# Optimization experiments

Hardware: AMD Instinct MI355X
Metric: run time of the kernel (lower is better)

The kernel has to match this reference:

```python
import jax, jax.numpy as jnp
import numpy as np

EMBED_DIM = 384
NUM_HEADS = 6
EPS = 1e-5

def _conv_proj(x, w_dw, gamma, beta, mean, var, stride):
    # x: [B,H,W,C]; depthwise 3x3 conv (groups=C), pad 1, then BN (inference), then flatten HW.
    C = x.shape[-1]
    y = jax.lax.conv_general_dilated(
        x, w_dw, window_strides=(stride, stride), padding=[(1, 1), (1, 1)],
        dimension_numbers=("NHWC", "HWIO", "NHWC"), feature_group_count=C)
    y = (y - mean) * jax.lax.rsqrt(var + EPS) * gamma + beta
    B, H, W, Cc = y.shape
    return y.reshape(B, H * W, Cc)

def _heads(x):
    # [B, L, C] -> [B, nH, L, hd]
    B, L, C = x.shape
    hd = C // NUM_HEADS
    return x.reshape(B, L, NUM_HEADS, hd).transpose(0, 2, 1, 3)

def setup_inputs() -> dict:
    key = jax.random.key(0)
    ks = jax.random.split(key, 20)
    B, H, W, C = 64, 28, 28, EMBED_DIM
    inp = {
        "hidden_state": jax.random.normal(ks[0], (B, 1 + H * W, C), dtype=jnp.float32),
        "height": H,
        "width": W,
    }
    std = 0.02
    for i, p in enumerate(("q", "k", "v")):
        inp[f"w_dw_{p}"] = jax.random.normal(ks[1 + i], (3, 3, 1, C), dtype=jnp.float32) * std
        inp[f"bn_gamma_{p}"] = jnp.ones((C,), jnp.float32) + 0.1 * jax.random.normal(ks[4 + i], (C,))
        inp[f"bn_beta_{p}"] = 0.1 * jax.random.normal(ks[7 + i], (C,))
        inp[f"bn_mean_{p}"] = 0.1 * jax.random.normal(ks[10 + i], (C,))
        inp[f"bn_var_{p}"] = jnp.ones((C,), jnp.float32) + 0.1 * jax.random.uniform(ks[13 + i], (C,))
        inp[f"W_{p}"] = jax.random.normal(ks[16 + i], (C, C), dtype=jnp.float32) * std
        inp[f"b_{p}"] = jnp.zeros((C,), jnp.float32)
    return inp

def reference(hidden_state, height, width,
              w_dw_q, bn_gamma_q, bn_beta_q, bn_mean_q, bn_var_q, W_q, b_q,
              w_dw_k, bn_gamma_k, bn_beta_k, bn_mean_k, bn_var_k, W_k, b_k,
              w_dw_v, bn_gamma_v, bn_beta_v, bn_mean_v, bn_var_v, W_v, b_v):
    B, _, C = hidden_state.shape
    scale = C ** (-0.5)  # note: embed_dim**-0.5, as in the source
    cls_token = hidden_state[:, :1]
    x = hidden_state[:, 1:].reshape(B, height, width, C)

    q = _conv_proj(x, w_dw_q, bn_gamma_q, bn_beta_q, bn_mean_q, bn_var_q, stride=1)
    k = _conv_proj(x, w_dw_k, bn_gamma_k, bn_beta_k, bn_mean_k, bn_var_k, stride=2)
    v = _conv_proj(x, w_dw_v, bn_gamma_v, bn_beta_v, bn_mean_v, bn_var_v, stride=2)

    q = jnp.concatenate((cls_token, q), axis=1)
    k = jnp.concatenate((cls_token, k), axis=1)
    v = jnp.concatenate((cls_token, v), axis=1)

    q = _heads(q @ W_q + b_q)  # [B,h,Lq,d]
    k = _heads(k @ W_k + b_k)  # [B,h,Lk,d]
    v = _heads(v @ W_v + b_v)

    scores = jnp.einsum("bhqd,bhkd->bhqk", q, k) * scale
    probs = jax.nn.softmax(scores, axis=-1)
    ctx = jnp.einsum("bhqk,bhkd->bhqd", probs, v)
    Lq = ctx.shape[2]
    return ctx.transpose(0, 2, 1, 3).reshape(B, Lq, C)
```

## Files before the change

### kernel.cpp

```cpp
#include <hip/hip_runtime.h>
#include <hip/hip_bf16.h>

#define C_DIM 384
#define BATCH 64
#define LQ 785
#define LK 197
#define NHEADS 6
#define HDIM 64
#define QTILES 785
#define KTILES 197
#define KPAD 208

typedef __hip_bfloat16 bf16;
typedef __attribute__((ext_vector_type(8))) short short8;
typedef __attribute__((ext_vector_type(4))) float float4v;

__device__ __forceinline__ float bf2f(bf16 x) { return __bfloat162float(x); }
__device__ __forceinline__ bf16 f2bf(float x) { return __float2bfloat16(x); }
__device__ __forceinline__ float lo16f(unsigned int u) { return __uint_as_float(u << 16); }
__device__ __forceinline__ float hi16f(unsigned int u) { return __uint_as_float(u & 0xffff0000u); }
__device__ __forceinline__ unsigned short bfb(float x) {
    union { bf16 h; unsigned short s; } u; u.h = f2bf(x); return u.s;
}
__device__ __forceinline__ unsigned int pk2(float a, float b) {
    return ((unsigned int)bfb(b) << 16) | bfb(a);
}

template<bool F32>
__device__ __forceinline__ float ldx(const void* p, size_t i) {
    if constexpr (F32) return ((const float*)p)[i];
    else return bf2f(((const bf16*)p)[i]);
}
template<bool F32>
__device__ __forceinline__ void stx(void* p, size_t i, float v) {
    if constexpr (F32) ((float*)p)[i] = v;
    else ((bf16*)p)[i] = f2bf(v);
}
template<bool F32>
__device__ __forceinline__ void ld4(const void* p, size_t i, float* o) {
    if constexpr (F32) {
        float4 v = *(const float4*)((const float*)p + i);
        o[0] = v.x; o[1] = v.y; o[2] = v.z; o[3] = v.w;
    } else {
        uint2 u = *(const uint2*)((const bf16*)p + i);
        o[0] = lo16f(u.x); o[1] = hi16f(u.x); o[2] = lo16f(u.y); o[3] = hi16f(u.y);
    }
}
template<bool F32>
__device__ __forceinline__ void ld2(const void* p, size_t i, float* o) {
    if constexpr (F32) {
        float2 v = *(const float2*)((const float*)p + i);
        o[0] = v.x; o[1] = v.y;
    } else {
        unsigned int u = *(const unsigned int*)((const bf16*)p + i);
        o[0] = lo16f(u); o[1] = hi16f(u);
    }
}

__global__ void detect_kernel(const void* varq, int* flag) {
    const unsigned short* u = (const unsigned short*)varq;
    int votes = 0;
    #pragma unroll
    for (int i = 0; i < 4; ++i) {
        float b = __uint_as_float(((unsigned int)u[2 * i]) << 16);
        votes += (b > 0.5f && b < 2.0f) ? 1 : 0;
    }
    *flag = (votes == 4) ? 1 : 0;
}

template<bool F32>
__global__ __launch_bounds__(256) void repack_kernel(const int* __restrict__ flagp,
    const void* __restrict__ W0, const void* __restrict__ W1, const void* __restrict__ W2,
    bf16* __restrict__ dst)
{
    if (*flagp != (F32 ? 0 : 1)) return;
    const void* W = blockIdx.y == 0 ? W0 : (blockIdx.y == 1 ? W1 : W2);
    bf16* d = dst + (size_t)blockIdx.y * (C_DIM * C_DIM);
    int idx = blockIdx.x * 256 + threadIdx.x;
    int k = idx / C_DIM, nc = idx - k * C_DIM;
    int nt = nc >> 4, n = nc & 15, kt = k >> 5, q = (k >> 3) & 3, j = k & 7;
    d[(size_t)((((nt * 12 + kt) * 4 + q) * 16 + n) * 8 + j)] = f2bf(ldx<F32>(W, idx));
}

template<bool F32>
__device__ __forceinline__ void foldw(const void* __restrict__ wdw,
    const void* __restrict__ gamma, const void* __restrict__ beta,
    const void* __restrict__ mean,  const void* __restrict__ var,
    int c0, float w[9][2], float sh[2])
{
    float g[2], be[2], mu[2], vv[2];
    ld2<F32>(gamma, c0, g); ld2<F32>(beta, c0, be);
    ld2<F32>(mean,  c0, mu); ld2<F32>(var,  c0, vv);
    float sc[2];
    #pragma unroll
    for (int i = 0; i < 2; ++i) {
        sc[i] = g[i] * rsqrtf(vv[i] + 1e-5f);
        sh[i] = be[i] - mu[i] * sc[i];
    }
    #pragma unroll
    for (int p = 0; p < 9; ++p) {
        float t[2];
        ld2<F32>(wdw, (size_t)p * C_DIM + c0, t);
        w[p][0] = t[0] * sc[0];
        w[p][1] = t[1] * sc[1];
    }
}

template<int OJH, bool F32>
__device__ __forceinline__ void conv_quad(int b, int oik, int c2,
    const void* __restrict__ hs,
    const void* wq_, const void* gq, const void* beq, const void* muq, const void* vaq,
    const void* wk_, const void* gk, const void* bek, const void* muk, const void* vak,
    const void* wv_, const void* gv, const void* bev, const void* muv, const void* vav,
    bf16* __restrict__ qa, bf16* __restrict__ ka, bf16* __restrict__ va)
{
    int c0 = c2 * 2;
    float wq[9][2], wk[9][2], wv[9][2], shq[2], shk[2], shv[2];
    foldw<F32>(wq_, gq, beq, muq, vaq, c0, wq, shq);
    foldw<F32>(wk_, gk, bek, muk, vak, c0, wk, shk);
    foldw<F32>(wv_, gv, bev, muv, vav, c0, wv, shv);

    size_t hb = (size_t)b * (LQ * C_DIM);
    int i0 = 2 * oik - 1;
    bool rv[4];
    #pragma unroll
    for (int ri = 0; ri < 4; ++ri) rv[ri] = ((unsigned)(i0 + ri)) < 28u;

    float xw[4][3][2];
    constexpr int JJ0 = 14 * OJH - 1;

    int rq0 = b * LQ + 1 + 2 * oik * 28;
    int rq1 = rq0 + 28;
    int rk  = b * LK + 1 + oik * 14;

    #pragma unroll
    for (int s = 0; s < 16; ++s) {
        const int jj = JJ0 + s;
        const int sl = ((jj % 3) + 3) % 3;
        const bool cval = (jj >= 0) && (jj < 28);
        #pragma unroll
        for (int ri = 0; ri < 4; ++ri) {
            if (cval && rv[ri])
                ld2<F32>(hs, hb + (size_t)(1 + (i0 + ri) * 28 + jj) * C_DIM + c0, xw[ri][sl]);
            else { xw[ri][sl][0] = 0.f; xw[ri][sl][1] = 0.f; }
        }
        if (s >= 2) {
            const int jc = jj - 1;
            float a0[2] = {}, a1[2] = {};
            #pragma unroll
            for (int di = 0; di < 3; ++di)
                #pragma unroll
                for (int dj = 0; dj < 3; ++dj) {
                    const int s2 = (((jc - 1 + dj) % 3) + 3) % 3;
                    const int t = di * 3 + dj;
                    a0[0] = fmaf(xw[di][s2][0],     wq[t][0], a0[0]);
                    a0[1] = fmaf(xw[di][s2][1],     wq[t][1], a0[1]);
                    a1[0] = fmaf(xw[di + 1][s2][0], wq[t][0], a1[0]);
                    a1[1] = fmaf(xw[di + 1][s2][1], wq[t][1], a1[1]);
                }
            *(unsigned int*)&qa[(size_t)(rq0 + jc) * C_DIM + c0] = pk2(a0[0] + shq[0], a0[1] + shq[1]);
            *(unsigned int*)&qa[(size_t)(rq1 + jc) * C_DIM + c0] = pk2(a1[0] + shq[0], a1[1] + shq[1]);
            if ((jc & 1) == 0) {
                float k0[2] = {}, v0[2] = {};
                #pragma unroll
                for (int di = 0; di < 3; ++di)
                    #pragma unroll
                    for (int dj = 0; dj < 3; ++dj) {
                        const int s2 = (((jc - 1 + dj) % 3) + 3) % 3;
                        const int t = di * 3 + dj;
                        k0[0] = fmaf(xw[di][s2][0], wk[t][0], k0[0]);
                        k0[1] = fmaf(xw[di][s2][1], wk[t][1], k0[1]);
                        v0[0] = fmaf(xw[di][s2][0], wv[t][0], v0[0]);
                        v0[1] = fmaf(xw[di][s2][1], wv[t][1], v0[1]);
                    }
                int ro = rk + (jc >> 1);
                *(unsigned int*)&ka[(size_t)ro * C_DIM + c0] = pk2(k0[0] + shk[0], k0[1] + shk[1]);
                *(unsigned int*)&va[(size_t)ro * C_DIM + c0] = pk2(v0[0] + shv[0], v0[1] + shv[1]);
            }
        }
    }
}

#define CONV4_BLOCKS 960
template<bool F32>
__global__ __launch_bounds__(384) void conv4_kernel(
    const int* __restrict__ flagp, const void* __restrict__ hs,
    const void* wq, const void* gq, const void* beq, const void* muq, const void* vaq,
    const void* wk, const void* gk, const void* bek, const void* muk, const void* vak,
    const void* wv, const void* gv, const void* bev, const void* muv, const void* vav,
    bf16* __restrict__ qa, bf16* __restrict__ ka, bf16* __restrict__ va)
{
    if (*flagp != (F32 ? 0 : 1)) return;
    int bid = blockIdx.x;
    int tid = threadIdx.x;
    if (bid < 896) {
        int w = (bid & 7) * 112 + (bid >> 3);
        int b = w / 14, oik = w - b * 14;
        int c2 = tid % 192, ojh = tid / 192;
        if (ojh == 0)
            conv_quad<0, F32>(b, oik, c2, hs, wq, gq, beq, muq, vaq,
                              wk, gk, bek, muk, vak, wv, gv, bev, muv, vav, qa, ka, va);
        else
            conv_quad<1, F32>(b, oik, c2, hs, wq, gq, beq, muq, vaq,
                              wk, gk, bek, muk, vak, wv, gv, bev, muv, vav, qa, ka, va);
    } else {
        int b = bid - 896;
        if (tid < 192) {
            int c0 = tid * 2;
            float v2[2];
            ld2<F32>(hs, (size_t)b * (LQ * C_DIM) + c0, v2);
            unsigned int pk = pk2(v2[0], v2[1]);
            *(unsigned int*)&qa[(size_t)(b * LQ) * C_DIM + c0] = pk;
            *(unsigned int*)&ka[(size_t)(b * LK) * C_DIM + c0] = pk;
            *(unsigned int*)&va[(size_t)(b * LK) * C_DIM + c0] = pk;
        }
    }
}

template<bool F32>
__global__ __launch_bounds__(512) void gemm_frag_kernel(
    const int* __restrict__ flagp,
    const bf16* __restrict__ qa, const bf16* __restrict__ ka, const bf16* __restrict__ va,
    const bf16* __restrict__ wrep,
    const void* __restrict__ b_q, const void* __restrict__ b_k, const void* __restrict__ b_v,
    void* __restrict__ outq, bf16* __restrict__ kbuf, bf16* __restrict__ vbuf)
{
    if (*flagp != (F32 ? 0 : 1)) return;

    int bidx = blockIdx.x;
    const bf16* A; const bf16* wr; const void* bias; int tile, mode;
    if (bidx < QTILES)                { mode = 0; tile = bidx;                  A = qa; wr = wrep;                          bias = b_q; }
    else if (bidx < QTILES + KTILES)  { mode = 1; tile = bidx - QTILES;         A = ka; wr = wrep + (size_t)C_DIM * C_DIM;     bias = b_k; }
    else                              { mode = 2; tile = bidx - QTILES - KTILES; A = va; wr = wrep + (size_t)2 * C_DIM * C_DIM; bias = b_v; }

    const bf16* Abase = A + (size_t)tile * (64 * C_DIM);
    const short8* wf = (const short8*)wr;
    int tid = threadIdx.x;
    int lane = tid & 63, wave = tid >> 6;
    int mrow = lane & 15, quad = lane >> 4;
    float4v acc[4][3] = {};

    #pragma unroll 2
    for (int kt = 0; kt < 12; ++kt) {
        short8 a[4];
        #pragma unroll
        for (int mt = 0; mt < 4; ++mt)
            a[mt] = *(const short8*)(Abase + (size_t)(mt * 16 + mrow) * C_DIM + (kt * 4 + quad) * 8);
        #pragma unroll
        for (int nt = 0; nt < 3; ++nt) {
            short8 bfrag = wf[(size_t)((wave * 3 + nt) * 12 + kt) * 64 + lane];
            #pragma unroll
            for (int mt = 0; mt < 4; ++mt)
                acc[mt][nt] = __builtin_amdgcn_mfma_f32_16x16x32_bf16(a[mt], bfrag, acc[mt][nt], 0, 0, 0);
        }
    }

    #pragma unroll
    for (int nt = 0; nt < 3; ++nt) {
        int col = wave * 48 + nt * 16 + mrow;
        float bb = ldx<F32>(bias, col);
        #pragma unroll
        for (int mt = 0; mt < 4; ++mt) {
            int row = tile * 64 + mt * 16 + quad * 4;
            #pragma unroll
            for (int r2 = 0; r2 < 4; ++r2) {
                float v = acc[mt][nt][r2] + bb;
                size_t o = (size_t)(row + r2) * C_DIM + col;
                if (mode == 0)      stx<F32>(outq, o, v);
                else if (mode == 1) kbuf[o] = f2bf(v);
                else                vbuf[o] = f2bf(v);
            }
        }
    }
}

__global__ __launch_bounds__(256) void vt_transpose_kernel(
    const bf16* __restrict__ v, bf16* __restrict__ vt)
{
    __shared__ unsigned short t[64][66];
    int bid = blockIdx.x;
    int ct = bid % 6; int tmp = bid / 6;
    int kt = tmp % 4; int b = tmp / 4;
    int k0 = kt * 64, c0 = ct * 64;
    int tid = threadIdx.x;

    for (int e = tid; e < 64 * 32; e += 256) {
        int r = e >> 5, c2 = e & 31;
        int k = k0 + r;
        unsigned int val = 0;
        if (k < LK) val = *(const unsigned int*)(v + ((size_t)b * LK + k) * C_DIM + c0 + c2 * 2);
        *(unsigned int*)&t[r][c2 * 2] = val;
    }
    __syncthreads();

    for (int e = tid; e < 64 * 32; e += 256) {
        int c = e >> 5, r2 = e & 31;
        int k = k0 + r2 * 2;
        if (k < KPAD) {
            unsigned int val = ((unsigned int)t[r2 * 2 + 1][c] << 16) | t[r2 * 2][c];
            *(unsigned int*)&vt[((size_t)(b * C_DIM + c0 + c)) * KPAD + k] = val;
        }
    }
}

template<int L, int OW, int STRIDE, bool F32, bool OF32>
__global__ __launch_bounds__(256) void fused_proj_kernel(
    const int* __restrict__ flagp,
    const void* __restrict__ hs, const void* __restrict__ wdw,
    const void* __restrict__ gamma, const void* __restrict__ beta,
    const void* __restrict__ mean,  const void* __restrict__ var,
    const bf16* __restrict__ Wrep,  const void* __restrict__ bias,
    void* __restrict__ O)
{
    if (*flagp != (F32 ? 0 : 1)) return;

    __shared__ bf16 A_s[64 * C_DIM];
    __shared__ float sc[C_DIM];
    __shared__ float sh[C_DIM];
    int tid = threadIdx.x;
    int m0 = blockIdx.x * 64;

    for (int c = tid; c < C_DIM; c += 256) {
        float s = ldx<F32>(gamma, c) * rsqrtf(ldx<F32>(var, c) + 1e-5f);
        sc[c] = s;
        sh[c] = ldx<F32>(beta, c) - ldx<F32>(mean, c) * s;
    }
    __syncthreads();

    for (int e = tid; e < 64 * 96; e += 256) {
        int m = e / 96;
        int c = (e - m * 96) * 4;
        int r = m0 + m;
        int b = r / L;
        int l = r - b * L;
        size_t hb = (size_t)b * (LQ * C_DIM);
        float v[4];
        if (l == 0) {
            ld4<F32>(hs, hb + c, v);
        } else {
            int p = l - 1;
            int oi = p / OW;
            int oj = p - oi * OW;
            float a0 = 0.f, a1 = 0.f, a2 = 0.f, a3 = 0.f;
            #pragma unroll
            for (int di = 0; di < 3; ++di) {
                int ii = oi * STRIDE - 1 + di;
                if (ii < 0 || ii >= 28) continue;
                #pragma unroll
                for (int dj = 0; dj < 3; ++dj) {
                    int jj = oj * STRIDE - 1 + dj;
                    if (jj < 0 || jj >= 28) continue;
                    float x[4], w[4];
                    ld4<F32>(hs, hb + (size_t)(1 + ii * 28 + jj) * C_DIM + c, x);
                    ld4<F32>(wdw, (size_t)(di * 3 + dj) * C_DIM + c, w);
                    a0 = fmaf(x[0], w[0], a0); a1 = fmaf(x[1], w[1], a1);
                    a2 = fmaf(x[2], w[2], a2); a3 = fmaf(x[3], w[3], a3);
                }
            }
            v[0] = a0 * sc[c + 0] + sh[c + 0];
            v[1] = a1 * sc[c + 1] + sh[c + 1];
            v[2] = a2 * sc[c + 2] + sh[c + 2];
            v[3] = a3 * sc[c + 3] + sh[c + 3];
        }
        int kt = c >> 5, q = (c >> 3) & 3, j = c & 7;
        int ofs = ((kt * 4 + q) * 64 + m) * 8 + j;
        ushort4 st = { bfb(v[0]), bfb(v[1]), bfb(v[2]), bfb(v[3]) };
        *(ushort4*)&A_s[ofs] = st;
    }
    __syncthreads();

    int lane = tid & 63, wave = tid >> 6;
    int mrow = lane & 15, quad = lane >> 4;
    float4v acc[4][6] = {};
    const short8* as = (const short8*)A_s;
    const short8* wr = (const short8*)Wrep;

    for (int kt = 0; kt < 12; ++kt) {
        short8 a[4];
        #pragma unroll
        for (int mt = 0; mt < 4; ++mt)
            a[mt] = as[(kt * 4 + quad) * 64 + mt * 16 + mrow];
        #pragma unroll
        for (int nt = 0; nt < 6; ++nt) {
            int ntg = wave * 6 + nt;
            short8 bfrag = wr[(size_t)(ntg * 12 + kt) * 64 + lane];
            #pragma unroll
            for (int mt = 0; mt < 4; ++mt)
                acc[mt][nt] = __builtin_amdgcn_mfma_f32_16x16x32_bf16(a[mt], bfrag, acc[mt][nt], 0, 0, 0);
        }
    }

    #pragma unroll
    for (int nt = 0; nt < 6; ++nt) {
        int col = wave * 96 + nt * 16 + mrow;
        float bb = ldx<F32>(bias, col);
        #pragma unroll
        for (int mt = 0; mt < 4; ++mt) {
            int row = m0 + mt * 16 + quad * 4;
            #pragma unroll
            for (int r2 = 0; r2 < 4; ++r2)
                stx<OF32>(O, (size_t)(row + r2) * C_DIM + col, acc[mt][nt][r2] + bb);
        }
    }
}

template<bool F32>
__global__ __launch_bounds__(256) void attn_vt_kernel(
    const int* __restrict__ flagp,
    const bf16* __restrict__ kg,
    const bf16* __restrict__ vt_g,
    void* __restrict__ qo)
{
    if (*flagp != (F32 ? 0 : 1)) return;

    __shared__ unsigned short Kf[8 * 2 * 64 * 8];
    __shared__ unsigned short Vt[64 * 128];
    __shared__ unsigned short Ps[4 * 16 * 128];

    int tid = threadIdx.x;
    int lane = tid & 63, wave = tid >> 6;
    int m = lane & 15, quad = lane >> 4;
    int bid = blockIdx.x;
    int qb = bid % 13;
    int bh = bid / 13;
    int h = bh % NHEADS, b = bh / NHEADS;
    int qbase = qb * 64 + wave * 16;

    int rev4m = ((m & 1) << 3) | ((m & 2) << 1) | ((m & 4) >> 1) | ((m & 8) >> 3);
    int revr[4];
    #pragma unroll
    for (int r = 0; r < 4; ++r) {
        int rr = quad * 4 + r;
        revr[r] = ((rr & 1) << 3) | ((rr & 2) << 1) | ((rr & 4) >> 1) | ((rr & 8) >> 3);
    }

    int qrow = min(qbase + m, LQ - 1);
    size_t qoff = ((size_t)b * LQ + qrow) * C_DIM + h * HDIM;
    short8 aq[2];
    #pragma unroll
    for (int ks = 0; ks < 2; ++ks) {
        float t[8];
        ld4<F32>(qo, qoff + ks * 32 + quad * 8, t);
        ld4<F32>(qo, qoff + ks * 32 + quad * 8 + 4, t + 4);
        short8 f;
        #pragma unroll
        for (int j = 0; j < 8; ++j) f[j] = (short)bfb(t[j]);
        aq[ks] = f;
    }

    const float scale = 0.05103103630798287f;
    float4v ctx[4] = {};
    float lsum4[4] = {};
    size_t kvbase = (size_t)b * LK * C_DIM + h * HDIM;
    size_t vtbase = (size_t)(b * C_DIM + h * HDIM) * KPAD;

    for (int c = 0; c < 2; ++c) {
        int c0 = c * 128;
        for (int e = tid; e < 1024; e += 256) {
            int col = e >> 3, d8 = e & 7;
            int gcol = c0 + col;
            uint4 val = {0, 0, 0, 0};
            if (gcol < LK) val = *(const uint4*)(kg + kvbase + (size_t)gcol * C_DIM + d8 * 8);
            int nt = col >> 4, n = col & 15, ks = d8 >> 2, q = d8 & 3;
            *(uint4*)&Kf[((nt * 2 + ks) * 64 + q * 16 + n) * 8] = val;
        }
        for (int e = tid; e < 1024; e += 256) {
            int d = e >> 4, kc = e & 15;
            uint4 val = {0, 0, 0, 0};
            if (c0 + kc * 8 < KPAD)
                val = *(const uint4*)(vt_g + vtbase + (size_t)d * KPAD + c0 + kc * 8);
            *(uint4*)&Vt[(d << 7) + ((kc ^ (d & 15)) << 3)] = val;
        }
        __syncthreads();

        const short8* kf = (const short8*)Kf;
        unsigned short* pw = Ps + wave * (16 * 128);
        int ntmax = (c == 0) ? 8 : 5;
        for (int nt = 0; nt < ntmax; ++nt) {
            float4v s = {0.f, 0.f, 0.f, 0.f};
            #pragma unroll
            for (int ks = 0; ks < 2; ++ks)
                s = __builtin_amdgcn_mfma_f32_16x16x32_bf16(aq[ks], kf[(nt * 2 + ks) * 64 + lane], s, 0, 0, 0);
            int coln = c0 + nt * 16 + m;
            bool valid = coln < LK;
            int chb = nt * 2 + (m >> 3);
            int sub = m & 7;
            #pragma unroll
            for (int r = 0; r < 4; ++r) {
                float pv = valid ? __expf(s[r] * scale) : 0.f;
                lsum4[r] += pv;
                pw[(((quad * 4 + r)) << 7) + ((chb ^ revr[r]) << 3) + sub] = bfb(pv);
            }
        }
        if (c == 1) {
            int sub = m & 7;
            #pragma unroll
            for (int nt = 5; nt < 8; ++nt) {
                int chb = nt * 2 + (m >> 3);
                #pragma unroll
                for (int r = 0; r < 4; ++r)
                    pw[(((quad * 4 + r)) << 7) + ((chb ^ revr[r]) << 3) + sub] = 0;
            }
        }

        const short8* vts = (const short8*)Vt;
        const short8* pf = (const short8*)Ps;
        #pragma unroll
        for (int ks = 0; ks < 4; ++ks) {
            short8 ap = pf[wave * 256 + (m << 4) + ((ks * 4 + quad) ^ rev4m)];
            #pragma unroll
            for (int ntv = 0; ntv < 4; ++ntv) {
                short8 bf_ = vts[((ntv * 16 + m) << 4) + ((ks * 4 + quad) ^ m)];
                ctx[ntv] = __builtin_amdgcn_mfma_f32_16x16x32_bf16(ap, bf_, ctx[ntv], 0, 0, 0);
            }
        }
        __syncthreads();
    }

    float inv[4];
    #pragma unroll
    for (int r = 0; r < 4; ++r) {
        float t = lsum4[r];
        t += __shfl_xor(t, 1);
        t += __shfl_xor(t, 2);
        t += __shfl_xor(t, 4);
        t += __shfl_xor(t, 8);
        inv[r] = 1.f / t;
    }
    #pragma unroll
    for (int ntv = 0; ntv < 4; ++ntv) {
        #pragma unroll
        for (int r = 0; r < 4; ++r) {
            int row = qbase + quad * 4 + r;
            if (row < LQ)
                stx<F32>(qo, ((size_t)b * LQ + row) * C_DIM + h * HDIM + ntv * 16 + m, ctx[ntv][r] * inv[r]);
        }
    }
}

template<bool F32>
__global__ __launch_bounds__(256) void attn_kernel(
    const int* __restrict__ flagp,
    const bf16* __restrict__ kg,
    const bf16* __restrict__ vg,
    void* __restrict__ qo)
{
    if (*flagp != (F32 ? 0 : 1)) return;

    __shared__ unsigned short Kf[8 * 2 * 64 * 8];
    __shared__ unsigned short Vf[4 * 4 * 64 * 8];
    __shared__ unsigned short Ps[4 * 16 * 136];

    int tid = threadIdx.x;
    int lane = tid & 63, wave = tid >> 6;
    int m = lane & 15, quad = lane >> 4;
    int bid = blockIdx.x;
    int qb = bid % 13;
    int bh = bid / 13;
    int h = bh % NHEADS, b = bh / NHEADS;
    int qbase = qb * 64 + wave * 16;

    int qrow = min(qbase + m, LQ - 1);
    size_t qoff = ((size_t)b * LQ + qrow) * C_DIM + h * HDIM;
    short8 aq[2];
    #pragma unroll
    for (int ks = 0; ks < 2; ++ks) {
        float t[8];
        ld4<F32>(qo, qoff + ks * 32 + quad * 8, t);
        ld4<F32>(qo, qoff + ks * 32 + quad * 8 + 4, t + 4);
        short8 f;
        #pragma unroll
        for (int j = 0; j < 8; ++j) f[j] = (short)bfb(t[j]);
        aq[ks] = f;
    }

    const float scale = 0.05103103630798287f;
    float4v ctx[4] = {};
    float lsum4[4] = {};
    size_t kvbase = (size_t)b * LK * C_DIM + h * HDIM;

    for (int c = 0; c < 2; ++c) {
        int c0 = c * 128;
        for (int e = tid; e < 1024; e += 256) {
            int col = e >> 3, d8 = e & 7;
            int gcol = c0 + col;
            uint4 val = {0, 0, 0, 0};
            if (gcol < LK) val = *(const uint4*)(kg + kvbase + (size_t)gcol * C_DIM + d8 * 8);
            int nt = col >> 4, n = col & 15, ks = d8 >> 2, q = d8 & 3;
            *(uint4*)&Kf[((nt * 2 + ks) * 64 + q * 16 + n) * 8] = val;
        }
        for (int e = tid; e < 1024; e += 256) {
            int p = e >> 3, d8 = e & 7;
            int gp = c0 + p;
            int ks = p >> 5, q = (p >> 3) & 3, j = p & 7;
            int ntv = d8 >> 1, nl0 = (d8 & 1) * 8;
            if (gp < LK) {
                union { uint4 u; unsigned short s[8]; } val;
                val.u = *(const uint4*)(vg + kvbase + (size_t)gp * C_DIM + d8 * 8);
                #pragma unroll
                for (int i = 0; i < 8; ++i)
                    Vf[((ntv * 4 + ks) * 64 + q * 16 + nl0 + i) * 8 + j] = val.s[i];
            } else {
                #pragma unroll
                for (int i = 0; i < 8; ++i)
                    Vf[((ntv * 4 + ks) * 64 + q * 16 + nl0 + i) * 8 + j] = 0;
            }
        }
        __syncthreads();

        const short8* kf = (const short8*)Kf;
        unsigned short* pw = Ps + wave * (16 * 136);
        int ntmax = (c == 0) ? 8 : 5;
        for (int nt = 0; nt < ntmax; ++nt) {
            float4v s = {0.f, 0.f, 0.f, 0.f};
            #pragma unroll
            for (int ks = 0; ks < 2; ++ks)
                s = __builtin_amdgcn_mfma_f32_16x16x32_bf16(aq[ks], kf[(nt * 2 + ks) * 64 + lane], s, 0, 0, 0);
            int coln = c0 + nt * 16 + m;
            bool valid = coln < LK;
            #pragma unroll
            for (int r = 0; r < 4; ++r) {
                float pv = valid ? __expf(s[r] * scale) : 0.f;
                lsum4[r] += pv;
                pw[(quad * 4 + r) * 136 + nt * 16 + m] = bfb(pv);
            }
        }
        if (c == 1) {
            #pragma unroll
            for (int nt = 5; nt < 8; ++nt)
                #pragma unroll
                for (int r = 0; r < 4; ++r)
                    pw[(quad * 4 + r) * 136 + nt * 16 + m] = 0;
        }

        const short8* vf = (const short8*)Vf;
        const short8* pf = (const short8*)Ps;
        #pragma unroll
        for (int ks = 0; ks < 4; ++ks) {
            short8 ap = pf[wave * 272 + m * 17 + ks * 4 + quad];
            #pragma unroll
            for (int ntv = 0; ntv < 4; ++ntv)
                ctx[ntv] = __builtin_amdgcn_mfma_f32_16x16x32_bf16(ap, vf[(ntv * 4 + ks) * 64 + lane], ctx[ntv], 0, 0, 0);
        }
        __syncthreads();
    }

    float inv[4];
    #pragma unroll
    for (int r = 0; r < 4; ++r) {
        float t = lsum4[r];
        t += __shfl_xor(t, 1);
        t += __shfl_xor(t, 2);
        t += __shfl_xor(t, 4);
        t += __shfl_xor(t, 8);
        inv[r] = 1.f / t;
    }
    #pragma unroll
    for (int ntv = 0; ntv < 4; ++ntv) {
        #pragma unroll
        for (int r = 0; r < 4; ++r) {
            int row = qbase + quad * 4 + r;
            if (row < LQ)
                stx<F32>(qo, ((size_t)b * LQ + row) * C_DIM + h * HDIM + ntv * 16 + m, ctx[ntv][r] * inv[r]);
        }
    }
}

extern "C" void kernel_launch(void* const* d_in, const int* in_sizes, int n_in,
                              void* d_out, int out_size, void* d_ws, size_t ws_size,
                              hipStream_t stream)
{
    const void* hs    = d_in[0];
    const void* wdw_q = d_in[3];
    const void* g_q   = d_in[4];
    const void* be_q  = d_in[5];
    const void* mu_q  = d_in[6];
    const void* va_q  = d_in[7];
    const void* W_q   = d_in[8];
    const void* b_q   = d_in[9];
    const void* wdw_k = d_in[10];
    const void* g_k   = d_in[11];
    const void* be_k  = d_in[12];
    const void* mu_k  = d_in[13];
    const void* va_k  = d_in[14];
    const void* W_k   = d_in[15];
    const void* b_k   = d_in[16];
    const void* wdw_v = d_in[17];
    const void* g_v   = d_in[18];
    const void* be_v  = d_in[19];
    const void* mu_v  = d_in[20];
    const void* va_v  = d_in[21];
    const void* W_v   = d_in[22];
    const void* b_v   = d_in[23];

    const size_t QA = (size_t)QTILES * 24576;
    const size_t KA = (size_t)KTILES * 24576;
    const size_t NEED_BIG = 16 + 2 * (3 * (size_t)C_DIM * C_DIM + QA + 4 * KA);

    int*  flag = (int*)d_ws;
    bf16* wrep = (bf16*)((char*)d_ws + 16);
    bf16* wrq  = wrep;
    bf16* wrk  = wrep + (size_t)C_DIM * C_DIM;
    bf16* wrv  = wrep + (size_t)2 * C_DIM * C_DIM;

    detect_kernel<<<1, 1, 0, stream>>>(va_q, flag);
    repack_kernel<false><<<dim3(576, 3), 256, 0, stream>>>(flag, W_q, W_k, W_v, wrep);
    repack_kernel<true ><<<dim3(576, 3), 256, 0, stream>>>(flag, W_q, W_k, W_v, wrep);

    if (ws_size >= NEED_BIG) {
        bf16* qa    = wrep + (size_t)3 * C_DIM * C_DIM;
        bf16* ka    = qa + QA;
        bf16* vaa   = ka + KA;
        bf16* kbuf  = vaa + KA;
        bf16* vbuf  = kbuf + KA;
        bf16* vbuft = qa;

        conv4_kernel<false><<<CONV4_BLOCKS, 384, 0, stream>>>(flag, hs,
            wdw_q, g_q, be_q, mu_q, va_q, wdw_k, g_k, be_k, mu_k, va_k,
            wdw_v, g_v, be_v, mu_v, va_v, qa, ka, vaa);
        conv4_kernel<true ><<<CONV4_BLOCKS, 384, 0, stream>>>(flag, hs,
            wdw_q, g_q, be_q, mu_q, va_q, wdw_k, g_k, be_k, mu_k, va_k,
            wdw_v, g_v, be_v, mu_v, va_v, qa, ka, vaa);

        gemm_frag_kernel<false><<<QTILES + 2 * KTILES, 512, 0, stream>>>(flag,
            qa, ka, vaa, wrep, b_q, b_k, b_v, d_out, kbuf, vbuf);
        gemm_frag_kernel<true ><<<QTILES + 2 * KTILES, 512, 0, stream>>>(flag,
            qa, ka, vaa, wrep, b_q, b_k, b_v, d_out, kbuf, vbuf);

        vt_transpose_kernel<<<BATCH * 24, 256, 0, stream>>>(vbuf, vbuft);

        attn_vt_kernel<false><<<384 * 13, 256, 0, stream>>>(flag, kbuf, vbuft, d_out);
        attn_vt_kernel<true ><<<384 * 13, 256, 0, stream>>>(flag, kbuf, vbuft, d_out);
    } else {
        bf16* kbuf = wrep + (size_t)3 * C_DIM * C_DIM;
        bf16* vbuf = kbuf + (size_t)BATCH * LK * C_DIM;

        fused_proj_kernel<LQ, 28, 1, false, false><<<LQ, 256, 0, stream>>>(flag, hs, wdw_q, g_q, be_q, mu_q, va_q, wrq, b_q, d_out);
        fused_proj_kernel<LQ, 28, 1, true,  true ><<<LQ, 256, 0, stream>>>(flag, hs, wdw_q, g_q, be_q, mu_q, va_q, wrq, b_q, d_out);
        fused_proj_kernel<LK, 14, 2, false, false><<<LK, 256, 0, stream>>>(flag, hs, wdw_k, g_k, be_k, mu_k, va_k, wrk, b_k, kbuf);
        fused_proj_kernel<LK, 14, 2, true,  false><<<LK, 256, 0, stream>>>(flag, hs, wdw_k, g_k, be_k, mu_k, va_k, wrk, b_k, kbuf);
        fused_proj_kernel<LK, 14, 2, false, false><<<LK, 256, 0, stream>>>(flag, hs, wdw_v, g_v, be_v, mu_v, va_v, wrv, b_v, vbuf);
        fused_proj_kernel<LK, 14, 2, true,  false><<<LK, 256, 0, stream>>>(flag, hs, wdw_v, g_v, be_v, mu_v, va_v, wrv, b_v, vbuf);

        attn_kernel<false><<<384 * 13, 256, 0, stream>>>(flag, kbuf, vbuf, d_out);
        attn_kernel<true ><<<384 * 13, 256, 0, stream>>>(flag, kbuf, vbuf, d_out);
    }
}
```

Measured before the change: 385.2 us.

## Stage GEMM A tile in swizzled LDS and merge dtype variants into one launch

Each 512-thread block now loads its 64x384 bf16 A tile into shared memory once, using a swizzled layout, before the MFMA loop. Previously all 8 waves re-read the same A fragments directly from global memory. The two templated launches (f32 and bf16 paths, one of which exited early) become a single launch that branches on the flag at runtime, removing one kernel launch. In exchange the kernel uses 48KB of LDS per block, which can limit how many blocks fit per CU, and adds a barrier.

```diff
diff --git a/kernel.cpp b/kernel.cpp
--- a/kernel.cpp
+++ b/kernel.cpp
@@ -217,16 +217,16 @@
     }
 }
 
-template<bool F32>
-__global__ __launch_bounds__(512) void gemm_frag_kernel(
+__global__ __launch_bounds__(512) void gemm_lds_kernel(
     const int* __restrict__ flagp,
     const bf16* __restrict__ qa, const bf16* __restrict__ ka, const bf16* __restrict__ va,
     const bf16* __restrict__ wrep,
     const void* __restrict__ b_q, const void* __restrict__ b_k, const void* __restrict__ b_v,
     void* __restrict__ outq, bf16* __restrict__ kbuf, bf16* __restrict__ vbuf)
 {
-    if (*flagp != (F32 ? 0 : 1)) return;
-
+    __shared__ bf16 A_s[64 * C_DIM];
+
+    const bool f32 = (*flagp == 0);
     int bidx = blockIdx.x;
     const bf16* A; const bf16* wr; const void* bias; int tile, mode;
     if (bidx < QTILES)                { mode = 0; tile = bidx;                  A = qa; wr = wrep;                          bias = b_q; }
@@ -234,10 +234,28 @@
     else                              { mode = 2; tile = bidx - QTILES - KTILES; A = va; wr = wrep + (size_t)2 * C_DIM * C_DIM; bias = b_v; }
 
     const bf16* Abase = A + (size_t)tile * (64 * C_DIM);
-    const short8* wf = (const short8*)wr;
     int tid = threadIdx.x;
     int lane = tid & 63, wave = tid >> 6;
     int mrow = lane & 15, quad = lane >> 4;
+
+    {
+        int l4 = lane & 3, l16 = lane >> 2;
+        #pragma unroll
+        for (int i = 0; i < 6; ++i) {
+            int t6 = wave * 6 + i;
+            int rbase = (t6 / 3) * 4;
+            int cbase = (t6 % 3) * 16;
+            int row = rbase + l4;
+            int ch  = cbase + l16;
+            uint4 v = *(const uint4*)(Abase + (size_t)row * C_DIM + ch * 8);
+            int dst = ch * 64 + (row ^ ((ch & 1) << 2));
+            *(uint4*)&A_s[dst * 8] = v;
+        }
+    }
+    __syncthreads();
+
+    const short8* as = (const short8*)A_s;
+    const short8* wf = (const short8*)wr;
     float4v acc[4][3] = {};
 
     #pragma unroll 2
@@ -245,7 +263,7 @@
         short8 a[4];
         #pragma unroll
         for (int mt = 0; mt < 4; ++mt)
-            a[mt] = *(const short8*)(Abase + (size_t)(mt * 16 + mrow) * C_DIM + (kt * 4 + quad) * 8);
+            a[mt] = as[(kt * 4 + quad) * 64 + ((mt * 16 + mrow) ^ ((quad & 1) << 2))];
         #pragma unroll
         for (int nt = 0; nt < 3; ++nt) {
             short8 bfrag = wf[(size_t)((wave * 3 + nt) * 12 + kt) * 64 + lane];
@@ -258,7 +276,7 @@
     #pragma unroll
     for (int nt = 0; nt < 3; ++nt) {
         int col = wave * 48 + nt * 16 + mrow;
-        float bb = ldx<F32>(bias, col);
+        float bb = f32 ? ((const float*)bias)[col] : bf2f(((const bf16*)bias)[col]);
         #pragma unroll
         for (int mt = 0; mt < 4; ++mt) {
             int row = tile * 64 + mt * 16 + quad * 4;
@@ -266,9 +284,14 @@
             for (int r2 = 0; r2 < 4; ++r2) {
                 float v = acc[mt][nt][r2] + bb;
                 size_t o = (size_t)(row + r2) * C_DIM + col;
-                if (mode == 0)      stx<F32>(outq, o, v);
-                else if (mode == 1) kbuf[o] = f2bf(v);
-                else                vbuf[o] = f2bf(v);
+                if (mode == 0) {
+                    if (f32) ((float*)outq)[o] = v;
+                    else     ((bf16*)outq)[o] = f2bf(v);
+                } else if (mode == 1) {
+                    kbuf[o] = f2bf(v);
+                } else {
+                    vbuf[o] = f2bf(v);
+                }
             }
         }
     }
@@ -722,9 +745,7 @@
             wdw_q, g_q, be_q, mu_q, va_q, wdw_k, g_k, be_k, mu_k, va_k,
             wdw_v, g_v, be_v, mu_v, va_v, qa, ka, vaa);
 
-        gemm_frag_kernel<false><<<QTILES + 2 * KTILES, 512, 0, stream>>>(flag,
-            qa, ka, vaa, wrep, b_q, b_k, b_v, d_out, kbuf, vbuf);
-        gemm_frag_kernel<true ><<<QTILES + 2 * KTILES, 512, 0, stream>>>(flag,
+        gemm_lds_kernel<<<QTILES + 2 * KTILES, 512, 0, stream>>>(flag,
             qa, ka, vaa, wrep, b_q, b_k, b_v, d_out, kbuf, vbuf);
 
         vt_transpose_kernel<<<BATCH * 24, 256, 0, stream>>>(vbuf, vbuft);
```

After: 355.2 us. 1.08x faster.
